# Kernel tuning notes

Measured on AMD Instinct MI355X. Metric: run time of the kernel, lower is better.

Reference implementation:

```python
import jax, jax.numpy as jnp
import numpy as np

NUM_HEADS = 12
DIM_HEAD = 32
EMBED_DIM = NUM_HEADS * DIM_HEAD  # 384
EPS = 1e-5


def _channel_layernorm(x, w, b):
    # LayerNorm over channel axis (axis=1) of [B, D, S, L], per spatial position
    mu = jnp.mean(x, axis=1, keepdims=True)
    var = jnp.mean(jnp.square(x - mu), axis=1, keepdims=True)
    xn = (x - mu) / jnp.sqrt(var + EPS)
    return xn * w[None, :, None, None] + b[None, :, None, None]


def _qkv(x, w, b):
    # 1x1 conv == per-position matmul: [3D, D] x [B, D, S, L] -> [B, 3D, S, L]
    B, D, S, L = x.shape
    y = jnp.einsum('od,bdsl->bosl', w, x) + b[None, :, None, None]
    q, k, v = jnp.split(y, 3, axis=1)
    shp = (B, NUM_HEADS, DIM_HEAD, S, L)
    return q.reshape(shp), k.reshape(shp), v.reshape(shp)


def setup_inputs() -> dict:
    key = jax.random.key(0)
    ks = jax.random.split(key, 5)
    B, D, S, L = 1, EMBED_DIM, 128, 256
    x = jax.random.normal(ks[0], (B, D, S, L), dtype=jnp.float32)
    row_w = jax.random.normal(ks[1], (3 * D, D), dtype=jnp.float32) * (D ** -0.5)
    row_b = jax.random.normal(ks[2], (3 * D,), dtype=jnp.float32) * 0.02
    col_w = jax.random.normal(ks[3], (3 * D, D), dtype=jnp.float32) * (D ** -0.5)
    col_b = jax.random.normal(ks[4], (3 * D,), dtype=jnp.float32) * 0.02
    return {
        'x': x,
        'row_w': row_w, 'row_b': row_b,
        'col_w': col_w, 'col_b': col_b,
        'ln1_w': jnp.ones((D,), jnp.float32), 'ln1_b': jnp.zeros((D,), jnp.float32),
        'ln2_w': jnp.ones((D,), jnp.float32), 'ln2_b': jnp.zeros((D,), jnp.float32),
    }


def reference(x, row_w, row_b, col_w, col_b, ln1_w, ln1_b, ln2_w, ln2_b):
    B, D, S, L = x.shape
    # --- row attention (attend across L within each row s) ---
    q, k, v = _qkv(x, row_w, row_b)  # [B,H,C,S,L]
    row_attn = jnp.einsum('bhcsi,bhcsj->bhsij', q, k)  # note: no 1/sqrt(d) scaling (faithful)
    row_attn = jax.nn.softmax(row_attn, axis=-1)
    row_out = jnp.einsum('bhsij,bhdsj->bhdsi', row_attn, v).reshape(B, D, S, L)
    out = _channel_layernorm(x + row_out, ln1_w, ln1_b)
    # --- column attention (attend across S within each column l) ---
    q, k, v = _qkv(out, col_w, col_b)
    col_attn = jnp.einsum('bhcil,bhcjl->bhijl', q, k)
    col_attn = jax.nn.softmax(col_attn, axis=-2)
    col_out = jnp.einsum('bhijl,bhdjl->bhdil', col_attn, v).reshape(B, D, S, L)
    out = _channel_layernorm(out + col_out, ln2_w, ln2_b)
    return out
```

## Files before the change

kernel.cpp:

```cpp
#include <hip/hip_runtime.h>
#include <math.h>

#define DCH 384
#define NH 12
#define CH 32
#define SS 128
#define LL 256
#define NPOS 32768
#define THREE_D 1152

typedef _Float16 f16_t;
typedef _Float16 f16x4 __attribute__((ext_vector_type(4)));
typedef _Float16 f16x8 __attribute__((ext_vector_type(8)));
typedef float f32x4 __attribute__((ext_vector_type(4)));

#define GLD16(gptr, lptr) __builtin_amdgcn_global_load_lds( \
    (const __attribute__((address_space(1))) unsigned int*)(gptr), \
    (__attribute__((address_space(3))) unsigned int*)(lptr), 16, 0, 0)

#define WAVE_LDS_FENCE() __asm__ volatile("s_waitcnt lgkmcnt(0)" ::: "memory")

__global__ __launch_bounds__(256) void conv_w(const float* __restrict__ in,
                                              f16_t* __restrict__ out, int n4) {
    int i = blockIdx.x * 256 + threadIdx.x;
    if (i < n4) {
        float4 v = ((const float4*)in)[i];
        unsigned short u0 = __builtin_bit_cast(unsigned short, (f16_t)v.x);
        unsigned short u1 = __builtin_bit_cast(unsigned short, (f16_t)v.y);
        unsigned short u2 = __builtin_bit_cast(unsigned short, (f16_t)v.z);
        unsigned short u3 = __builtin_bit_cast(unsigned short, (f16_t)v.w);
        uint2 r;
        r.x = (unsigned)u0 | ((unsigned)u1 << 16);
        r.y = (unsigned)u2 | ((unsigned)u3 << 16);
        ((uint2*)out)[i] = r;
    }
}

__global__ __launch_bounds__(256) void conv_xT(const float* __restrict__ in,
                                               f16_t* __restrict__ outp) {
    __shared__ float tile[64][65];
    const int p0 = blockIdx.x * 64;
    const int k0 = blockIdx.y * 64;
    const int tx = threadIdx.x & 63, ty = threadIdx.x >> 6;
#pragma unroll
    for (int i = 0; i < 16; ++i)
        tile[ty * 16 + i][tx] = in[(size_t)(k0 + ty * 16 + i) * NPOS + p0 + tx];
    __syncthreads();
    const int pr = threadIdx.x >> 2;
    const int cg = threadIdx.x & 3;
    union { uint4 v[2]; unsigned int u[8]; } res;
#pragma unroll
    for (int j = 0; j < 8; ++j) {
        unsigned short lo = __builtin_bit_cast(unsigned short, (f16_t)tile[cg * 16 + 2 * j][pr]);
        unsigned short hi = __builtin_bit_cast(unsigned short, (f16_t)tile[cg * 16 + 2 * j + 1][pr]);
        res.u[j] = (unsigned)lo | ((unsigned)hi << 16);
    }
    uint4* dst = (uint4*)&outp[(size_t)(p0 + pr) * DCH + k0 + cg * 16];
    dst[0] = res.v[0];
    dst[1] = res.v[1];
}

__global__ __launch_bounds__(256) void qkv_gemm_f16(
        const f16_t* __restrict__ Wh,
        const float* __restrict__ bias,
        const f16_t* __restrict__ Xp,
        f16_t* __restrict__ Yq, f16_t* __restrict__ Yk, f16_t* __restrict__ Yv)
{
    __shared__ f16_t sha[2][128 * 32];
    __shared__ f16_t shb[2][128 * 32];
    const int tid  = threadIdx.x;
    const int lane = tid & 63;
    const int wave = tid >> 6;

    const int hwid = blockIdx.y * 9 + blockIdx.x;
    const int nid  = (hwid & 7) * 288 + (hwid >> 3);
    const int ot   = nid % 9;
    const int pt   = nid / 9;
    const int o0 = ot * 128;
    const int p0 = pt * 128;
    const int wr = wave >> 1, wc = wave & 1;

    f32x4 acc[4][4] = {};

    const int c0 = wave * 128 + lane;
    const int c1 = c0 + 64;
    const int r0 = c0 >> 2, r1 = c1 >> 2;
    const int kg0 = (c0 & 3) ^ ((r0 >> 1) & 3);
    const int kg1 = (c1 & 3) ^ ((r1 >> 1) & 3);
    const f16_t* ga0 = Wh + (size_t)(o0 + r0) * DCH + kg0 * 8;
    const f16_t* ga1 = Wh + (size_t)(o0 + r1) * DCH + kg1 * 8;
    const f16_t* gb0 = Xp + (size_t)(p0 + r0) * DCH + kg0 * 8;
    const f16_t* gb1 = Xp + (size_t)(p0 + r1) * DCH + kg1 * 8;
    const int lofA0 = (wave * 128) * 8;
    const int lofA1 = (wave * 128 + 64) * 8;

    const int mrow = lane & 15;
    const int kgq  = lane >> 4;
    const int kgr8 = (kgq ^ ((mrow >> 1) & 3)) * 8;

    GLD16(ga0, &sha[0][lofA0]);
    GLD16(ga1, &sha[0][lofA1]);
    GLD16(gb0, &shb[0][lofA0]);
    GLD16(gb1, &shb[0][lofA1]);
    __syncthreads();

    constexpr int NK = DCH / 32;
#pragma unroll
    for (int t = 0; t < NK; ++t) {
        const int cur = t & 1;
        const int nxt = cur ^ 1;
        if (t < NK - 1) {
            const int kk = (t + 1) * 32;
            GLD16(ga0 + kk, &sha[nxt][lofA0]);
            GLD16(ga1 + kk, &sha[nxt][lofA1]);
            GLD16(gb0 + kk, &shb[nxt][lofA0]);
            GLD16(gb1 + kk, &shb[nxt][lofA1]);
        }
        f16x8 af[4], bfr[4];
#pragma unroll
        for (int mi = 0; mi < 4; ++mi)
            af[mi] = *(const f16x8*)(&sha[cur][(wr * 64 + mi * 16 + mrow) * 32 + kgr8]);
#pragma unroll
        for (int ni = 0; ni < 4; ++ni)
            bfr[ni] = *(const f16x8*)(&shb[cur][(wc * 64 + ni * 16 + mrow) * 32 + kgr8]);
#pragma unroll
        for (int mi = 0; mi < 4; ++mi)
#pragma unroll
            for (int ni = 0; ni < 4; ++ni)
                acc[mi][ni] = __builtin_amdgcn_mfma_f32_16x16x32_f16(
                    af[mi], bfr[ni], acc[mi][ni], 0, 0, 0);
        __syncthreads();
    }

    const int col = lane & 15;
    const int rq4 = (lane >> 4) * 4;
    const int qkv = ot / 3;
    const int grp = ot % 3;

    if (qkv < 2) {
        f16_t* Yt = (qkv == 0) ? Yq : Yk;
#pragma unroll
        for (int mi = 0; mi < 4; ++mi) {
            const int h  = grp * 4 + wr * 2 + (mi >> 1);
            const int cb = (mi & 1) * 16 + rq4;
            const int ob = o0 + wr * 64 + mi * 16 + rq4;
            const float b0 = bias[ob], b1 = bias[ob + 1];
            const float b2 = bias[ob + 2], b3 = bias[ob + 3];
#pragma unroll
            for (int ni = 0; ni < 4; ++ni) {
                const int p = p0 + wc * 64 + ni * 16 + col;
                union { uint2 u; f16_t h4[4]; } w;
                w.h4[0] = (f16_t)(acc[mi][ni][0] + b0);
                w.h4[1] = (f16_t)(acc[mi][ni][1] + b1);
                w.h4[2] = (f16_t)(acc[mi][ni][2] + b2);
                w.h4[3] = (f16_t)(acc[mi][ni][3] + b3);
                *(uint2*)(Yt + ((size_t)h * NPOS + p) * CH + cb) = w.u;
            }
        }
    } else {
#pragma unroll
        for (int mi = 0; mi < 4; ++mi) {
#pragma unroll
            for (int r = 0; r < 4; ++r) {
                const int cg = grp * 128 + wr * 64 + mi * 16 + rq4 + r;
                const float br = bias[768 + cg];
#pragma unroll
                for (int ni = 0; ni < 4; ++ni) {
                    const int p = p0 + wc * 64 + ni * 16 + col;
                    Yv[(size_t)cg * NPOS + p] = (f16_t)(acc[mi][ni][r] + br);
                }
            }
        }
    }
}

template <int SEQ, bool XT16>
__global__ __launch_bounds__(256) void mfma_attn(
        const f16_t* __restrict__ Yq, const f16_t* __restrict__ Yk,
        const f16_t* __restrict__ Yv, const void* __restrict__ Xv_,
        float* __restrict__ R)
{
    constexpr int JT  = SEQ / 16;
    constexpr int NIT = SEQ / 64;
    constexpr int PST = SEQ + 8;
    constexpr int VST = SEQ + 8;
    __shared__ f16_t Ks[SEQ * CH];
    __shared__ f16_t Vs[CH * VST];
    __shared__ f16_t pb[4][16 * PST];
    const int tid  = threadIdx.x;
    const int lane = tid & 63;
    const int wave = tid >> 6;
    const int col = lane & 15, quad = lane >> 4;
    const int h = blockIdx.x % NH;
    const size_t pbase = (size_t)(blockIdx.x / NH) * SEQ;

    const f16_t* qg = Yq + ((size_t)h * NPOS + pbase) * CH;
    const f16_t* kg = Yk + ((size_t)h * NPOS + pbase) * CH;
    const f16_t* vg = Yv + (size_t)h * CH * NPOS + pbase;
    f16_t* mypb = pb[wave];

    {
        const int ksw = (lane & 3) ^ ((lane >> 3) & 3);
        const int lrow32 = (lane >> 2) * 32;
#pragma unroll
        for (int i = 0; i < SEQ / 64; ++i) {
            const int off = (wave * (SEQ / 64) + i) * 512;
            GLD16(kg + off + lrow32 + ksw * 8, Ks + off);
        }
    }
    {
        constexpr int CPR = SEQ / 8;
        const int vch = tid % CPR;
        const int vr0 = tid / CPR;
#pragma unroll
        for (int r = vr0; r < CH; r += 256 / CPR)
            *(float4*)(Vs + r * VST + vch * 8) =
                *(const float4*)(vg + (size_t)r * NPOS + vch * 8);
    }
    __syncthreads();

    const int kq8 = (quad ^ ((col >> 1) & 3)) * 8;

    for (int it = 0; it < NIT; ++it) {
        const int i0 = (wave * NIT + it) * 16;
        const f16x8 qf = *(const f16x8*)(qg + (size_t)(i0 + col) * CH + quad * 8);
        f32x4 st[JT];
#pragma unroll
        for (int mt = 0; mt < JT; ++mt) {
            f16x8 kf = *(const f16x8*)(Ks + (mt * 16 + col) * CH + kq8);
            st[mt] = __builtin_amdgcn_mfma_f32_16x16x32_f16(kf, qf, (f32x4){0.f, 0.f, 0.f, 0.f}, 0, 0, 0);
        }
        float sum = 0.f;
#pragma unroll
        for (int mt = 0; mt < JT; ++mt)
#pragma unroll
            for (int r = 0; r < 4; ++r) {
                st[mt][r] = __expf(st[mt][r]);
                sum += st[mt][r];
            }
        sum += __shfl_xor(sum, 16, 64);
        sum += __shfl_xor(sum, 32, 64);
        const float inv = 1.f / sum;
#pragma unroll
        for (int mt = 0; mt < JT; ++mt) {
            union { uint2 u; f16_t h4[4]; } w;
            w.h4[0] = (f16_t)(st[mt][0] * inv);
            w.h4[1] = (f16_t)(st[mt][1] * inv);
            w.h4[2] = (f16_t)(st[mt][2] * inv);
            w.h4[3] = (f16_t)(st[mt][3] * inv);
            *(uint2*)(mypb + col * PST + mt * 16 + quad * 4) = w.u;
        }
        WAVE_LDS_FENCE();

        f32x4 o0a = {0.f, 0.f, 0.f, 0.f}, o0b = {0.f, 0.f, 0.f, 0.f};
        f32x4 o1a = {0.f, 0.f, 0.f, 0.f}, o1b = {0.f, 0.f, 0.f, 0.f};
#pragma unroll
        for (int ks = 0; ks < SEQ / 32; ks += 2) {
            f16x8 pf0 = *(const f16x8*)(mypb + col * PST + ks * 32 + quad * 8);
            f16x8 pf1 = *(const f16x8*)(mypb + col * PST + (ks + 1) * 32 + quad * 8);
            f16x8 va0 = *(const f16x8*)(Vs + col * VST + ks * 32 + quad * 8);
            f16x8 va1 = *(const f16x8*)(Vs + col * VST + (ks + 1) * 32 + quad * 8);
            f16x8 vb0 = *(const f16x8*)(Vs + (16 + col) * VST + ks * 32 + quad * 8);
            f16x8 vb1 = *(const f16x8*)(Vs + (16 + col) * VST + (ks + 1) * 32 + quad * 8);
            o0a = __builtin_amdgcn_mfma_f32_16x16x32_f16(va0, pf0, o0a, 0, 0, 0);
            o0b = __builtin_amdgcn_mfma_f32_16x16x32_f16(va1, pf1, o0b, 0, 0, 0);
            o1a = __builtin_amdgcn_mfma_f32_16x16x32_f16(vb0, pf0, o1a, 0, 0, 0);
            o1b = __builtin_amdgcn_mfma_f32_16x16x32_f16(vb1, pf1, o1b, 0, 0, 0);
        }
        const f32x4 ot0 = o0a + o0b;
        const f32x4 ot1 = o1a + o1b;

        const size_t pos = pbase + i0 + col;
        if constexpr (XT16) {
            const f16_t* Xh = (const f16_t*)Xv_;
            const f16x4 xa = *(const f16x4*)(Xh + pos * DCH + h * CH + quad * 4);
            const f16x4 xb = *(const f16x4*)(Xh + pos * DCH + h * CH + 16 + quad * 4);
#pragma unroll
            for (int r = 0; r < 4; ++r) {
                R[(size_t)(h * CH + quad * 4 + r) * NPOS + pos]      = (float)xa[r] + ot0[r];
                R[(size_t)(h * CH + 16 + quad * 4 + r) * NPOS + pos] = (float)xb[r] + ot1[r];
            }
        } else {
            const float* Xf = (const float*)Xv_;
#pragma unroll
            for (int r = 0; r < 4; ++r) {
                const size_t c0r = (size_t)(h * CH + quad * 4 + r) * NPOS + pos;
                const size_t c1r = (size_t)(h * CH + 16 + quad * 4 + r) * NPOS + pos;
                R[c0r] = Xf[c0r] + ot0[r];
                R[c1r] = Xf[c1r] + ot1[r];
            }
        }
    }
}

__global__ __launch_bounds__(256) void ln_stats(const float* __restrict__ A,
                                                float* __restrict__ mu,
                                                float* __restrict__ rs) {
    __shared__ float ssum[4][64], ssq[4][64];
    const int i = threadIdx.x & 63;
    const int g = threadIdx.x >> 6;
    const int p = blockIdx.x * 64 + i;
    float sum = 0.f, sq = 0.f;
    const float* ap = A + (size_t)(g * 96) * NPOS + p;
#pragma unroll 4
    for (int d = 0; d < 96; ++d) {
        float v = ap[(size_t)d * NPOS];
        sum += v;
        sq += v * v;
    }
    ssum[g][i] = sum;
    ssq[g][i] = sq;
    __syncthreads();
    if (g == 0) {
        float s = ssum[0][i] + ssum[1][i] + ssum[2][i] + ssum[3][i];
        float q = ssq[0][i] + ssq[1][i] + ssq[2][i] + ssq[3][i];
        float m = s * (1.f / DCH);
        float var = q * (1.f / DCH) - m * m;
        mu[p] = m;
        rs[p] = rsqrtf(var + 1e-5f);
    }
}

__global__ __launch_bounds__(256) void norm_xT(
        const float* __restrict__ A, const float* __restrict__ mu,
        const float* __restrict__ rs, const float* __restrict__ w,
        const float* __restrict__ b, f16_t* __restrict__ Xp) {
    __shared__ float tile[64][65];
    const int l0 = (blockIdx.x & 3) * 64;
    const int s  = (blockIdx.x >> 2) & (SS - 1);
    const int k0 = (blockIdx.x >> 9) * 64;
    const int tx = threadIdx.x & 63, ty = threadIdx.x >> 6;
    const int pos0 = s * LL + l0;
#pragma unroll
    for (int i = 0; i < 16; ++i) {
        const int d = k0 + ty * 16 + i;
        float v = A[(size_t)d * NPOS + pos0 + tx];
        tile[ty * 16 + i][tx] = (v - mu[pos0 + tx]) * rs[pos0 + tx] * w[d] + b[d];
    }
    __syncthreads();
    const int pr = threadIdx.x >> 2;
    const int cg = threadIdx.x & 3;
    union { uint4 v[2]; unsigned int u[8]; } res;
#pragma unroll
    for (int j = 0; j < 8; ++j) {
        unsigned short lo = __builtin_bit_cast(unsigned short, (f16_t)tile[cg * 16 + 2 * j][pr]);
        unsigned short hi = __builtin_bit_cast(unsigned short, (f16_t)tile[cg * 16 + 2 * j + 1][pr]);
        res.u[j] = (unsigned)lo | ((unsigned)hi << 16);
    }
    uint4* dst = (uint4*)&Xp[(size_t)((l0 + pr) * SS + s) * DCH + k0 + cg * 16];
    dst[0] = res.v[0];
    dst[1] = res.v[1];
}

__global__ __launch_bounds__(256) void norm_transpose(
        const float* __restrict__ in, const float* __restrict__ mu,
        const float* __restrict__ rs, const float* __restrict__ w,
        const float* __restrict__ b, float* __restrict__ out, int Rr, int Cc) {
    __shared__ float tile[32][33];
    const int ntc = Cc >> 5, ntr = Rr >> 5;
    int tc = blockIdx.x % ntc;
    int tr = (blockIdx.x / ntc) % ntr;
    int d = blockIdx.x / (ntc * ntr);
    int tx = threadIdx.x & 31, ty = threadIdx.x >> 5;
    const float* ip = in + (size_t)d * Rr * Cc;
    float* op = out + (size_t)d * Rr * Cc;
    const float wd = w[d], bd = b[d];
#pragma unroll
    for (int i = 0; i < 32; i += 8) {
        const int r = tr * 32 + ty + i;
        const int c = tc * 32 + tx;
        const int pos = r * Cc + c;
        float v = ip[(size_t)r * Cc + c];
        tile[ty + i][tx] = (v - mu[pos]) * rs[pos] * wd + bd;
    }
    __syncthreads();
#pragma unroll
    for (int i = 0; i < 32; i += 8)
        op[(size_t)(tc * 32 + ty + i) * Rr + tr * 32 + tx] = tile[tx][ty + i];
}

extern "C" void kernel_launch(void* const* d_in, const int* in_sizes, int n_in,
                              void* d_out, int out_size, void* d_ws, size_t ws_size,
                              hipStream_t stream) {
    const float* x     = (const float*)d_in[0];
    const float* row_w = (const float*)d_in[1];
    const float* row_b = (const float*)d_in[2];
    const float* col_w = (const float*)d_in[3];
    const float* col_b = (const float*)d_in[4];
    const float* ln1_w = (const float*)d_in[5];
    const float* ln1_b = (const float*)d_in[6];
    const float* ln2_w = (const float*)d_in[7];
    const float* ln2_b = (const float*)d_in[8];
    float* out = (float*)d_out;

    char* ws = (char*)d_ws;
    const size_t ysz = (size_t)NH * NPOS * CH * 2;
    const size_t abytes = (size_t)DCH * NPOS * 4;
    f16_t* Yq = (f16_t*)ws;
    f16_t* Yk = (f16_t*)(ws + ysz);
    f16_t* Yv = (f16_t*)(ws + 2 * ysz);
    float* A  = (float*)(ws + 3 * ysz);
    f16_t* Xp = (f16_t*)(ws + 3 * ysz + abytes);
    f16_t* Wh = (f16_t*)(ws + 3 * ysz + abytes + ysz);
    float* MU = (float*)(ws + 3 * ysz + abytes + ysz + (1 << 21));
    float* RS = MU + NPOS;

    dim3 ggrid(THREE_D / 128, NPOS / 128);
    const int wn4 = THREE_D * DCH / 4;
    dim3 cgrid(NPOS / 64, DCH / 64);

    conv_w<<<(wn4 + 255) / 256, 256, 0, stream>>>(row_w, Wh, wn4);
    conv_xT<<<cgrid, 256, 0, stream>>>(x, Xp);
    qkv_gemm_f16<<<ggrid, 256, 0, stream>>>(Wh, row_b, Xp, Yq, Yk, Yv);
    mfma_attn<LL, false><<<NH * SS, 256, 0, stream>>>(Yq, Yk, Yv, x, A);
    ln_stats<<<NPOS / 64, 256, 0, stream>>>(A, MU, RS);
    norm_xT<<<(DCH / 64) * SS * (LL / 64), 256, 0, stream>>>(A, MU, RS, ln1_w, ln1_b, Xp);

    conv_w<<<(wn4 + 255) / 256, 256, 0, stream>>>(col_w, Wh, wn4);
    qkv_gemm_f16<<<ggrid, 256, 0, stream>>>(Wh, col_b, Xp, Yq, Yk, Yv);
    mfma_attn<SS, true><<<NH * LL, 256, 0, stream>>>(Yq, Yk, Yv, Xp, A);
    ln_stats<<<NPOS / 64, 256, 0, stream>>>(A, MU, RS);
    norm_transpose<<<DCH * (LL / 32) * (SS / 32), 256, 0, stream>>>(
        A, MU, RS, ln2_w, ln2_b, out, LL, SS);
}
```

Measured before the change: 351.8 us.

## Restructure QKV GEMM: full-K weight tile in LDS, activations streamed via registers

The QKV GEMM now loads the whole 128x384 f16 weight tile into LDS once, using a swizzled layout, and runs 8 waves per block over 256 positions. Each wave streams its activation fragments from global memory straight into registers with a 3-deep prefetch. This removes the per-k-step barrier and the double-buffered LDS staging. The cost is 96KB of LDS per block, which lowers occupancy, and B loads that are exposed to global latency without LDS reuse.

```diff
diff --git a/kernel.cpp b/kernel.cpp
--- a/kernel.cpp
+++ b/kernel.cpp
@@ -60,76 +60,67 @@
     dst[1] = res.v[1];
 }
 
-__global__ __launch_bounds__(256) void qkv_gemm_f16(
+__global__ __launch_bounds__(512) void qkv_gemm_f16(
         const f16_t* __restrict__ Wh,
         const float* __restrict__ bias,
         const f16_t* __restrict__ Xp,
         f16_t* __restrict__ Yq, f16_t* __restrict__ Yk, f16_t* __restrict__ Yv)
 {
-    __shared__ f16_t sha[2][128 * 32];
-    __shared__ f16_t shb[2][128 * 32];
+    __shared__ f16_t sha[128 * 384];
     const int tid  = threadIdx.x;
     const int lane = tid & 63;
     const int wave = tid >> 6;
 
     const int hwid = blockIdx.y * 9 + blockIdx.x;
-    const int nid  = (hwid & 7) * 288 + (hwid >> 3);
+    const int nid  = (hwid & 7) * 144 + (hwid >> 3);
     const int ot   = nid % 9;
     const int pt   = nid / 9;
     const int o0 = ot * 128;
-    const int p0 = pt * 128;
-    const int wr = wave >> 1, wc = wave & 1;
-
-    f32x4 acc[4][4] = {};
-
-    const int c0 = wave * 128 + lane;
-    const int c1 = c0 + 64;
-    const int r0 = c0 >> 2, r1 = c1 >> 2;
-    const int kg0 = (c0 & 3) ^ ((r0 >> 1) & 3);
-    const int kg1 = (c1 & 3) ^ ((r1 >> 1) & 3);
-    const f16_t* ga0 = Wh + (size_t)(o0 + r0) * DCH + kg0 * 8;
-    const f16_t* ga1 = Wh + (size_t)(o0 + r1) * DCH + kg1 * 8;
-    const f16_t* gb0 = Xp + (size_t)(p0 + r0) * DCH + kg0 * 8;
-    const f16_t* gb1 = Xp + (size_t)(p0 + r1) * DCH + kg1 * 8;
-    const int lofA0 = (wave * 128) * 8;
-    const int lofA1 = (wave * 128 + 64) * 8;
+    const int p0 = pt * 256;
 
     const int mrow = lane & 15;
     const int kgq  = lane >> 4;
-    const int kgr8 = (kgq ^ ((mrow >> 1) & 3)) * 8;
-
-    GLD16(ga0, &sha[0][lofA0]);
-    GLD16(ga1, &sha[0][lofA1]);
-    GLD16(gb0, &shb[0][lofA0]);
-    GLD16(gb1, &shb[0][lofA1]);
-    __syncthreads();
-
+
+#pragma unroll
+    for (int j = 0; j < 12; ++j) {
+        const int ibase = (wave * 12 + j) * 64;
+        const int i = ibase + lane;
+        const int row = i / 48;
+        const int s = i - row * 48;
+        const int g = s ^ (row & 7);
+        GLD16(Wh + (size_t)(o0 + row) * DCH + g * 8, sha + (size_t)ibase * 8);
+    }
+
+    const f16_t* bp0 = Xp + (size_t)(p0 + wave * 32 + mrow) * DCH + kgq * 8;
+    const f16_t* bp1 = bp0 + (size_t)16 * DCH;
+
+    f32x4 acc[8][2] = {};
+    f16x8 breg[3][2];
+
+    breg[0][0] = *(const f16x8*)(bp0);
+    breg[0][1] = *(const f16x8*)(bp1);
+    breg[1][0] = *(const f16x8*)(bp0 + 32);
+    breg[1][1] = *(const f16x8*)(bp1 + 32);
+
+    __syncthreads();
+
+    const int key = mrow & 7;
     constexpr int NK = DCH / 32;
 #pragma unroll
     for (int t = 0; t < NK; ++t) {
-        const int cur = t & 1;
-        const int nxt = cur ^ 1;
-        if (t < NK - 1) {
-            const int kk = (t + 1) * 32;
-            GLD16(ga0 + kk, &sha[nxt][lofA0]);
-            GLD16(ga1 + kk, &sha[nxt][lofA1]);
-            GLD16(gb0 + kk, &shb[nxt][lofA0]);
-            GLD16(gb1 + kk, &shb[nxt][lofA1]);
-        }
-        f16x8 af[4], bfr[4];
-#pragma unroll
-        for (int mi = 0; mi < 4; ++mi)
-            af[mi] = *(const f16x8*)(&sha[cur][(wr * 64 + mi * 16 + mrow) * 32 + kgr8]);
-#pragma unroll
-        for (int ni = 0; ni < 4; ++ni)
-            bfr[ni] = *(const f16x8*)(&shb[cur][(wc * 64 + ni * 16 + mrow) * 32 + kgr8]);
-#pragma unroll
-        for (int mi = 0; mi < 4; ++mi)
-#pragma unroll
-            for (int ni = 0; ni < 4; ++ni)
-                acc[mi][ni] = __builtin_amdgcn_mfma_f32_16x16x32_f16(
-                    af[mi], bfr[ni], acc[mi][ni], 0, 0, 0);
-        __syncthreads();
+        if (t + 2 < NK) {
+            breg[(t + 2) % 3][0] = *(const f16x8*)(bp0 + (t + 2) * 32);
+            breg[(t + 2) % 3][1] = *(const f16x8*)(bp1 + (t + 2) * 32);
+        }
+        const int soff = ((t * 4 + kgq) ^ key) * 8;
+#pragma unroll
+        for (int mi = 0; mi < 8; ++mi) {
+            const f16x8 a = *(const f16x8*)(sha + (size_t)(mi * 16 + mrow) * DCH + soff);
+            acc[mi][0] = __builtin_amdgcn_mfma_f32_16x16x32_f16(
+                a, breg[t % 3][0], acc[mi][0], 0, 0, 0);
+            acc[mi][1] = __builtin_amdgcn_mfma_f32_16x16x32_f16(
+                a, breg[t % 3][1], acc[mi][1], 0, 0, 0);
+        }
     }
 
     const int col = lane & 15;
@@ -140,15 +131,15 @@
     if (qkv < 2) {
         f16_t* Yt = (qkv == 0) ? Yq : Yk;
 #pragma unroll
-        for (int mi = 0; mi < 4; ++mi) {
-            const int h  = grp * 4 + wr * 2 + (mi >> 1);
+        for (int mi = 0; mi < 8; ++mi) {
+            const int h  = grp * 4 + (mi >> 1);
             const int cb = (mi & 1) * 16 + rq4;
-            const int ob = o0 + wr * 64 + mi * 16 + rq4;
+            const int ob = o0 + mi * 16 + rq4;
             const float b0 = bias[ob], b1 = bias[ob + 1];
             const float b2 = bias[ob + 2], b3 = bias[ob + 3];
 #pragma unroll
-            for (int ni = 0; ni < 4; ++ni) {
-                const int p = p0 + wc * 64 + ni * 16 + col;
+            for (int ni = 0; ni < 2; ++ni) {
+                const int p = p0 + wave * 32 + ni * 16 + col;
                 union { uint2 u; f16_t h4[4]; } w;
                 w.h4[0] = (f16_t)(acc[mi][ni][0] + b0);
                 w.h4[1] = (f16_t)(acc[mi][ni][1] + b1);
@@ -159,14 +150,14 @@
         }
     } else {
 #pragma unroll
-        for (int mi = 0; mi < 4; ++mi) {
+        for (int mi = 0; mi < 8; ++mi) {
 #pragma unroll
             for (int r = 0; r < 4; ++r) {
-                const int cg = grp * 128 + wr * 64 + mi * 16 + rq4 + r;
+                const int cg = grp * 128 + mi * 16 + rq4 + r;
                 const float br = bias[768 + cg];
 #pragma unroll
-                for (int ni = 0; ni < 4; ++ni) {
-                    const int p = p0 + wc * 64 + ni * 16 + col;
+                for (int ni = 0; ni < 2; ++ni) {
+                    const int p = p0 + wave * 32 + ni * 16 + col;
                     Yv[(size_t)cg * NPOS + p] = (f16_t)(acc[mi][ni][r] + br);
                 }
             }
@@ -405,19 +396,19 @@
     float* MU = (float*)(ws + 3 * ysz + abytes + ysz + (1 << 21));
     float* RS = MU + NPOS;
 
-    dim3 ggrid(THREE_D / 128, NPOS / 128);
+    dim3 ggrid(THREE_D / 128, NPOS / 256);
     const int wn4 = THREE_D * DCH / 4;
     dim3 cgrid(NPOS / 64, DCH / 64);
 
     conv_w<<<(wn4 + 255) / 256, 256, 0, stream>>>(row_w, Wh, wn4);
     conv_xT<<<cgrid, 256, 0, stream>>>(x, Xp);
-    qkv_gemm_f16<<<ggrid, 256, 0, stream>>>(Wh, row_b, Xp, Yq, Yk, Yv);
+    qkv_gemm_f16<<<ggrid, 512, 0, stream>>>(Wh, row_b, Xp, Yq, Yk, Yv);
     mfma_attn<LL, false><<<NH * SS, 256, 0, stream>>>(Yq, Yk, Yv, x, A);
     ln_stats<<<NPOS / 64, 256, 0, stream>>>(A, MU, RS);
     norm_xT<<<(DCH / 64) * SS * (LL / 64), 256, 0, stream>>>(A, MU, RS, ln1_w, ln1_b, Xp);
 
     conv_w<<<(wn4 + 255) / 256, 256, 0, stream>>>(col_w, Wh, wn4);
-    qkv_gemm_f16<<<ggrid, 256, 0, stream>>>(Wh, col_b, Xp, Yq, Yk, Yv);
+    qkv_gemm_f16<<<ggrid, 512, 0, stream>>>(Wh, col_b, Xp, Yq, Yk, Yv);
     mfma_attn<SS, true><<<NH * LL, 256, 0, stream>>>(Yq, Yk, Yv, Xp, A);
     ln_stats<<<NPOS / 64, 256, 0, stream>>>(A, MU, RS);
     norm_transpose<<<DCH * (LL / 32) * (SS / 32), 256, 0, stream>>>(
```

Result: faster. 342.8 us (-2.6%).
